# Performance work log

Measured on AMD Instinct MI355X. Metric: run time of the kernel, lower is better.

Reference implementation:

```python
import jax, jax.numpy as jnp
import numpy as np

R = 2            # interleaving factor (init kwarg r)
C = 16           # feature channels
N = 500_000      # number of sparse voxels
GRID = 256       # fine-grid extent per axis


def setup_inputs() -> dict:
    key = jax.random.key(0)
    kc, kf = jax.random.split(key)
    coords = jax.random.randint(kc, (N, 3), 0, GRID, dtype=jnp.int32)
    feats = jax.random.normal(kf, (N, C), dtype=jnp.float32)
    return {"feats": feats, "coords": coords}


def reference(feats, coords):
    # Sparse interleaving: group fine voxels into coarse voxels of size R^3,
    # scattering each point's C features into the slot given by its intra-cell offset.
    r2 = R * R
    r3 = r2 * R
    n = coords.shape[0]
    base = coords // R                      # [N,3] coarse voxel coords
    off = coords % R                        # [N,3] intra-cell offset
    offset_idx = off[:, 0] * r2 + off[:, 1] * R + off[:, 2]  # [N]

    # jit-compatible unique: fixed output size (worst case: all points distinct)
    unique_coords, inv = jnp.unique(base, axis=0, size=n, fill_value=-1,
                                    return_inverse=True)
    inv = inv.reshape(-1)                   # [N] row in aggregated output

    # target column = offset_idx*C + channel  (matches torch scatter_ layout)
    col = offset_idx[:, None] * C + jnp.arange(C, dtype=offset_idx.dtype)[None, :]  # [N,C]
    agg = jnp.zeros((n, C * r3), dtype=feats.dtype)
    agg = agg.at[inv[:, None], col].set(feats)
    return unique_coords.astype(jnp.int32), agg
```

## Files before the change

### kernel.cpp

```cpp
#include <hip/hip_runtime.h>


#define WORDS 65536u

__global__ void mark_kernel(const int* __restrict__ coords,
                            unsigned* __restrict__ bitmap, int n) {
    int i = blockIdx.x * 256 + threadIdx.x;
    if (i >= n) return;
    int cx = coords[3 * i], cy = coords[3 * i + 1], cz = coords[3 * i + 2];
    unsigned key = ((unsigned)(cx >> 1) << 14) | ((unsigned)(cy >> 1) << 7) |
                   (unsigned)(cz >> 1);
    atomicOr(&bitmap[key >> 5], 1u << (key & 31));
}

__global__ void scanall_kernel(const unsigned* __restrict__ bitmap,
                               unsigned* __restrict__ chunkExcl,
                               unsigned* __restrict__ U) {
    __shared__ unsigned sh[256];
    int t = threadIdx.x;
    unsigned s = 0;
    unsigned base = (unsigned)t * 256u;
#pragma unroll 8
    for (unsigned j = 0; j < 256u; ++j) s += __popc(bitmap[base + j]);
    unsigned x = s;
    sh[t] = x; __syncthreads();
    for (int d = 1; d < 256; d <<= 1) {
        unsigned y = (t >= d) ? sh[t - d] : 0u;
        __syncthreads();
        x += y; sh[t] = x; __syncthreads();
    }
    chunkExcl[t] = x - s;
    if (t == 255) *U = x;
}

__global__ void rank_coords_pad_kernel(const unsigned* __restrict__ bitmap,
                                       const unsigned* __restrict__ chunkExcl,
                                       const unsigned* __restrict__ U,
                                       unsigned* __restrict__ rank_base,
                                       float* __restrict__ coords_out, int n) {
    __shared__ unsigned sh[256];
    int t = threadIdx.x;
    unsigned w = blockIdx.x * 256 + t;
    unsigned word = bitmap[w];
    unsigned cnt = __popc(word);
    unsigned x = cnt;
    sh[t] = x; __syncthreads();
    for (int d = 1; d < 256; d <<= 1) {
        unsigned y = (t >= d) ? sh[t - d] : 0u;
        __syncthreads();
        x += y; sh[t] = x; __syncthreads();
    }
    unsigned rb = chunkExcl[blockIdx.x] + x - cnt;
    rank_base[w] = rb;
    while (word) {
        int k = __ffs(word) - 1;
        word &= word - 1;
        unsigned cell = w * 32u + (unsigned)k;
        coords_out[3 * rb + 0] = (float)(cell >> 14);
        coords_out[3 * rb + 1] = (float)((cell >> 7) & 127u);
        coords_out[3 * rb + 2] = (float)(cell & 127u);
        ++rb;
    }
    unsigned u = *U;
    int nthreads = gridDim.x * 256;
    for (unsigned i = u + w; i < (unsigned)n; i += nthreads) {
        coords_out[3 * i + 0] = -1.0f;
        coords_out[3 * i + 1] = -1.0f;
        coords_out[3 * i + 2] = -1.0f;
    }
}

__global__ void winner_kernel(const int* __restrict__ coords,
                              const unsigned* __restrict__ bitmap,
                              const unsigned* __restrict__ rank_base,
                              int* __restrict__ winner, int n) {
    int i = blockIdx.x * 256 + threadIdx.x;
    if (i >= n) return;
    int cx = coords[3 * i], cy = coords[3 * i + 1], cz = coords[3 * i + 2];
    unsigned key = ((unsigned)(cx >> 1) << 14) | ((unsigned)(cy >> 1) << 7) |
                   (unsigned)(cz >> 1);
    unsigned off = ((unsigned)(cx & 1) << 2) | ((unsigned)(cy & 1) << 1) |
                   (unsigned)(cz & 1);
    unsigned wd = key >> 5;
    unsigned r = rank_base[wd] + __popc(bitmap[wd] & ((1u << (key & 31)) - 1u));
    atomicMax(&winner[r * 8u + off], i);
}

__global__ void gather_kernel(const float* __restrict__ feats,
                              const int* __restrict__ winner,
                              float* __restrict__ agg, int total4) {
    int j = blockIdx.x * 256 + threadIdx.x;
    if (j >= total4) return;
    int slot = j >> 2;
    int c4 = j & 3;
    int w = winner[slot];
    float4 v = make_float4(0.f, 0.f, 0.f, 0.f);
    if (w >= 0) v = ((const float4*)feats)[(size_t)w * 4 + c4];
    ((float4*)agg)[j] = v;
}

extern "C" void kernel_launch(void* const* d_in, const int* in_sizes, int n_in,
                              void* d_out, int out_size, void* d_ws, size_t ws_size,
                              hipStream_t stream) {
    const float* feats = (const float*)d_in[0];
    const int* coords  = (const int*)d_in[1];
    int n = in_sizes[1] / 3;

    float* out        = (float*)d_out;
    float* coords_out = out;
    float* agg        = out + (size_t)3 * n;

    unsigned* bitmap    = (unsigned*)d_ws;
    unsigned* rank_base = bitmap + WORDS;
    unsigned* chunkExcl = rank_base + WORDS;
    unsigned* U         = chunkExcl + 256;
    int*      winner    = (int*)(U + 4);

    (void)hipMemsetAsync(bitmap, 0, WORDS * sizeof(unsigned), stream);

    int nb = (n + 255) / 256;
    mark_kernel<<<nb, 256, 0, stream>>>(coords, bitmap, n);
    scanall_kernel<<<1, 256, 0, stream>>>(bitmap, chunkExcl, U);
    rank_coords_pad_kernel<<<WORDS / 256, 256, 0, stream>>>(bitmap, chunkExcl, U,
                                                            rank_base, coords_out, n);
    winner_kernel<<<nb, 256, 0, stream>>>(coords, bitmap, rank_base, winner, n);
    int total4 = n * 32;
    gather_kernel<<<(total4 + 255) / 256, 256, 0, stream>>>(feats, winner, agg,
                                                            total4);
}
```

Before: 373.9 us.

## Fuse all interleave stages into one persistent kernel with grid barriers

Replaces the five separate launches (mark, scan, rank/coords, winner, gather) with one persistent kernel of 1024 blocks. The stages are separated by atomic-counter grid barriers, and all loops become grid-stride. The per-chunk popcount reduction is now spread over 256 blocks instead of one block doing a serial 256-word loop. This removes inter-kernel launch gaps and the single-block scan bottleneck. In exchange it relies on all 1024 blocks being co-resident for the spin barriers to avoid deadlock, and adds barrier synchronisation cost.

```diff
diff --git a/kernel.cpp b/kernel.cpp
--- a/kernel.cpp
+++ b/kernel.cpp
@@ -1,102 +1,128 @@
 #include <hip/hip_runtime.h>
 
 
-#define WORDS 65536u
+#define WORDS   65536u
+#define NBLK    1024u
+#define NTHREAD (NBLK * 256u)
 
-__global__ void mark_kernel(const int* __restrict__ coords,
-                            unsigned* __restrict__ bitmap, int n) {
-    int i = blockIdx.x * 256 + threadIdx.x;
-    if (i >= n) return;
-    int cx = coords[3 * i], cy = coords[3 * i + 1], cz = coords[3 * i + 2];
-    unsigned key = ((unsigned)(cx >> 1) << 14) | ((unsigned)(cy >> 1) << 7) |
-                   (unsigned)(cz >> 1);
-    atomicOr(&bitmap[key >> 5], 1u << (key & 31));
+__device__ __forceinline__ void gridbar(unsigned* ctr) {
+    __threadfence();
+    __syncthreads();
+    if (threadIdx.x == 0) {
+        atomicAdd(ctr, 1u);
+        while (__hip_atomic_load(ctr, __ATOMIC_ACQUIRE,
+                                 __HIP_MEMORY_SCOPE_AGENT) < NBLK)
+            __builtin_amdgcn_s_sleep(8);
+    }
+    __syncthreads();
+    __threadfence();
 }
 
-__global__ void scanall_kernel(const unsigned* __restrict__ bitmap,
-                               unsigned* __restrict__ chunkExcl,
-                               unsigned* __restrict__ U) {
+__global__ __launch_bounds__(256, 4)
+void interleave_fused(const float* __restrict__ feats,
+                      const int* __restrict__ coords,
+                      unsigned* __restrict__ ctrs,
+                      unsigned* __restrict__ bitmap,
+                      unsigned* __restrict__ chunkExcl,
+                      unsigned* __restrict__ Uptr,
+                      unsigned* __restrict__ rank_base,
+                      int* __restrict__ winner,
+                      float* __restrict__ coords_out,
+                      float* __restrict__ agg,
+                      int n) {
     __shared__ unsigned sh[256];
-    int t = threadIdx.x;
-    unsigned s = 0;
-    unsigned base = (unsigned)t * 256u;
-#pragma unroll 8
-    for (unsigned j = 0; j < 256u; ++j) s += __popc(bitmap[base + j]);
-    unsigned x = s;
-    sh[t] = x; __syncthreads();
-    for (int d = 1; d < 256; d <<= 1) {
-        unsigned y = (t >= d) ? sh[t - d] : 0u;
+    const int t   = threadIdx.x;
+    const int b   = blockIdx.x;
+    const int gid = b * 256 + t;
+
+    for (int i = gid; i < n; i += NTHREAD) {
+        int cx = coords[3 * i], cy = coords[3 * i + 1], cz = coords[3 * i + 2];
+        unsigned key = ((unsigned)(cx >> 1) << 14) | ((unsigned)(cy >> 1) << 7) |
+                       (unsigned)(cz >> 1);
+        atomicOr(&bitmap[key >> 5], 1u << (key & 31));
+    }
+    gridbar(&ctrs[0]);
+
+    if (b < 256) {
+        sh[t] = __popc(bitmap[b * 256 + t]);
         __syncthreads();
-        x += y; sh[t] = x; __syncthreads();
+        for (int d = 128; d > 0; d >>= 1) {
+            if (t < d) sh[t] += sh[t + d];
+            __syncthreads();
+        }
+        if (t == 0) chunkExcl[b] = sh[0];
     }
-    chunkExcl[t] = x - s;
-    if (t == 255) *U = x;
-}
+    gridbar(&ctrs[1]);
 
-__global__ void rank_coords_pad_kernel(const unsigned* __restrict__ bitmap,
-                                       const unsigned* __restrict__ chunkExcl,
-                                       const unsigned* __restrict__ U,
-                                       unsigned* __restrict__ rank_base,
-                                       float* __restrict__ coords_out, int n) {
-    __shared__ unsigned sh[256];
-    int t = threadIdx.x;
-    unsigned w = blockIdx.x * 256 + t;
-    unsigned word = bitmap[w];
-    unsigned cnt = __popc(word);
-    unsigned x = cnt;
-    sh[t] = x; __syncthreads();
-    for (int d = 1; d < 256; d <<= 1) {
-        unsigned y = (t >= d) ? sh[t - d] : 0u;
-        __syncthreads();
-        x += y; sh[t] = x; __syncthreads();
+    if (b == 0) {
+        unsigned s = chunkExcl[t];
+        unsigned x = s;
+        sh[t] = x; __syncthreads();
+        for (int d = 1; d < 256; d <<= 1) {
+            unsigned y = (t >= d) ? sh[t - d] : 0u;
+            __syncthreads();
+            x += y; sh[t] = x; __syncthreads();
+        }
+        chunkExcl[t] = x - s;
+        if (t == 255) *Uptr = x;
     }
-    unsigned rb = chunkExcl[blockIdx.x] + x - cnt;
-    rank_base[w] = rb;
-    while (word) {
-        int k = __ffs(word) - 1;
-        word &= word - 1;
-        unsigned cell = w * 32u + (unsigned)k;
-        coords_out[3 * rb + 0] = (float)(cell >> 14);
-        coords_out[3 * rb + 1] = (float)((cell >> 7) & 127u);
-        coords_out[3 * rb + 2] = (float)(cell & 127u);
-        ++rb;
+    gridbar(&ctrs[2]);
+
+    if (b < 256) {
+        unsigned w = b * 256 + t;
+        unsigned word = bitmap[w];
+        unsigned cnt = __popc(word);
+        unsigned x = cnt;
+        sh[t] = x; __syncthreads();
+        for (int d = 1; d < 256; d <<= 1) {
+            unsigned y = (t >= d) ? sh[t - d] : 0u;
+            __syncthreads();
+            x += y; sh[t] = x; __syncthreads();
+        }
+        unsigned rb = chunkExcl[b] + x - cnt;
+        rank_base[w] = rb;
+        while (word) {
+            int k = __ffs(word) - 1;
+            word &= word - 1;
+            unsigned cell = w * 32u + (unsigned)k;
+            coords_out[3 * rb + 0] = (float)(cell >> 14);
+            coords_out[3 * rb + 1] = (float)((cell >> 7) & 127u);
+            coords_out[3 * rb + 2] = (float)(cell & 127u);
+            ++rb;
+        }
     }
-    unsigned u = *U;
-    int nthreads = gridDim.x * 256;
-    for (unsigned i = u + w; i < (unsigned)n; i += nthreads) {
-        coords_out[3 * i + 0] = -1.0f;
-        coords_out[3 * i + 1] = -1.0f;
-        coords_out[3 * i + 2] = -1.0f;
+    {
+        unsigned u = *Uptr;
+        for (unsigned i = u + gid; i < (unsigned)n; i += NTHREAD) {
+            coords_out[3 * i + 0] = -1.0f;
+            coords_out[3 * i + 1] = -1.0f;
+            coords_out[3 * i + 2] = -1.0f;
+        }
     }
-}
+    gridbar(&ctrs[3]);
 
-__global__ void winner_kernel(const int* __restrict__ coords,
-                              const unsigned* __restrict__ bitmap,
-                              const unsigned* __restrict__ rank_base,
-                              int* __restrict__ winner, int n) {
-    int i = blockIdx.x * 256 + threadIdx.x;
-    if (i >= n) return;
-    int cx = coords[3 * i], cy = coords[3 * i + 1], cz = coords[3 * i + 2];
-    unsigned key = ((unsigned)(cx >> 1) << 14) | ((unsigned)(cy >> 1) << 7) |
-                   (unsigned)(cz >> 1);
-    unsigned off = ((unsigned)(cx & 1) << 2) | ((unsigned)(cy & 1) << 1) |
-                   (unsigned)(cz & 1);
-    unsigned wd = key >> 5;
-    unsigned r = rank_base[wd] + __popc(bitmap[wd] & ((1u << (key & 31)) - 1u));
-    atomicMax(&winner[r * 8u + off], i);
-}
+    for (int i = gid; i < n; i += NTHREAD) {
+        int cx = coords[3 * i], cy = coords[3 * i + 1], cz = coords[3 * i + 2];
+        unsigned key = ((unsigned)(cx >> 1) << 14) | ((unsigned)(cy >> 1) << 7) |
+                       (unsigned)(cz >> 1);
+        unsigned off = ((unsigned)(cx & 1) << 2) | ((unsigned)(cy & 1) << 1) |
+                       (unsigned)(cz & 1);
+        unsigned wd = key >> 5;
+        unsigned r = rank_base[wd] +
+                     __popc(bitmap[wd] & ((1u << (key & 31)) - 1u));
+        atomicMax(&winner[r * 8u + off], i);
+    }
+    gridbar(&ctrs[4]);
 
-__global__ void gather_kernel(const float* __restrict__ feats,
-                              const int* __restrict__ winner,
-                              float* __restrict__ agg, int total4) {
-    int j = blockIdx.x * 256 + threadIdx.x;
-    if (j >= total4) return;
-    int slot = j >> 2;
-    int c4 = j & 3;
-    int w = winner[slot];
-    float4 v = make_float4(0.f, 0.f, 0.f, 0.f);
-    if (w >= 0) v = ((const float4*)feats)[(size_t)w * 4 + c4];
-    ((float4*)agg)[j] = v;
+    int total4 = n * 32;
+    for (int j = gid; j < total4; j += NTHREAD) {
+        int slot = j >> 2;
+        int c4 = j & 3;
+        int w = winner[slot];
+        float4 v = make_float4(0.f, 0.f, 0.f, 0.f);
+        if (w >= 0) v = ((const float4*)feats)[(size_t)w * 4 + c4];
+        ((float4*)agg)[j] = v;
+    }
 }
 
 extern "C" void kernel_launch(void* const* d_in, const int* in_sizes, int n_in,
@@ -110,21 +136,16 @@
     float* coords_out = out;
     float* agg        = out + (size_t)3 * n;
 
-    unsigned* bitmap    = (unsigned*)d_ws;
-    unsigned* rank_base = bitmap + WORDS;
-    unsigned* chunkExcl = rank_base + WORDS;
+    unsigned* ctrs      = (unsigned*)d_ws;
+    unsigned* bitmap    = ctrs + 8;
+    unsigned* chunkExcl = bitmap + WORDS;
     unsigned* U         = chunkExcl + 256;
-    int*      winner    = (int*)(U + 4);
+    unsigned* rank_base = U + 4;
+    int*      winner    = (int*)(rank_base + WORDS);
 
-    (void)hipMemsetAsync(bitmap, 0, WORDS * sizeof(unsigned), stream);
+    (void)hipMemsetAsync(ctrs, 0, (8 + WORDS) * sizeof(unsigned), stream);
 
-    int nb = (n + 255) / 256;
-    mark_kernel<<<nb, 256, 0, stream>>>(coords, bitmap, n);
-    scanall_kernel<<<1, 256, 0, stream>>>(bitmap, chunkExcl, U);
-    rank_coords_pad_kernel<<<WORDS / 256, 256, 0, stream>>>(bitmap, chunkExcl, U,
-                                                            rank_base, coords_out, n);
-    winner_kernel<<<nb, 256, 0, stream>>>(coords, bitmap, rank_base, winner, n);
-    int total4 = n * 32;
-    gather_kernel<<<(total4 + 255) / 256, 256, 0, stream>>>(feats, winner, agg,
-                                                            total4);
+    interleave_fused<<<NBLK, 256, 0, stream>>>(feats, coords, ctrs, bitmap,
+                                               chunkExcl, U, rank_base, winner,
+                                               coords_out, agg, n);
 }
```

After: 1.350 ms. 261% more time.

## Replace per-slot gather with memset plus per-point scatter of winning features

Applied to the files above, without the earlier changes.

The final stage no longer gathers over every output slot. The whole aggregated output is zeroed with a bulk memset. Then a per-point kernel recomputes each point's slot and copies its 64-byte feature row only when it is the winning writer. This drops the full read of the winner array and the per-slot branching. In exchange it adds a second pass of coords, bitmap and rank lookups plus scattered 64-byte writes on top of the full-size memset.

```diff
diff --git a/kernel.cpp b/kernel.cpp
--- a/kernel.cpp
+++ b/kernel.cpp
@@ -86,17 +86,26 @@
     atomicMax(&winner[r * 8u + off], i);
 }
 
-__global__ void gather_kernel(const float* __restrict__ feats,
-                              const int* __restrict__ winner,
-                              float* __restrict__ agg, int total4) {
-    int j = blockIdx.x * 256 + threadIdx.x;
-    if (j >= total4) return;
-    int slot = j >> 2;
-    int c4 = j & 3;
-    int w = winner[slot];
-    float4 v = make_float4(0.f, 0.f, 0.f, 0.f);
-    if (w >= 0) v = ((const float4*)feats)[(size_t)w * 4 + c4];
-    ((float4*)agg)[j] = v;
+__global__ void scatter_kernel(const float* __restrict__ feats,
+                               const int* __restrict__ coords,
+                               const unsigned* __restrict__ bitmap,
+                               const unsigned* __restrict__ rank_base,
+                               const int* __restrict__ winner,
+                               float* __restrict__ agg, int n) {
+    int i = blockIdx.x * 256 + threadIdx.x;
+    if (i >= n) return;
+    int cx = coords[3 * i], cy = coords[3 * i + 1], cz = coords[3 * i + 2];
+    unsigned key = ((unsigned)(cx >> 1) << 14) | ((unsigned)(cy >> 1) << 7) |
+                   (unsigned)(cz >> 1);
+    unsigned off = ((unsigned)(cx & 1) << 2) | ((unsigned)(cy & 1) << 1) |
+                   (unsigned)(cz & 1);
+    unsigned wd = key >> 5;
+    unsigned r = rank_base[wd] + __popc(bitmap[wd] & ((1u << (key & 31)) - 1u));
+    unsigned slot = r * 8u + off;
+    if (winner[slot] != i) return;
+    const float4* src = (const float4*)(feats + (size_t)i * 16);
+    float4* dst = (float4*)(agg + (size_t)slot * 16u);
+    dst[0] = src[0]; dst[1] = src[1]; dst[2] = src[2]; dst[3] = src[3];
 }
 
 extern "C" void kernel_launch(void* const* d_in, const int* in_sizes, int n_in,
@@ -117,6 +126,7 @@
     int*      winner    = (int*)(U + 4);
 
     (void)hipMemsetAsync(bitmap, 0, WORDS * sizeof(unsigned), stream);
+    (void)hipMemsetAsync(agg, 0, (size_t)128 * n * sizeof(float), stream);
 
     int nb = (n + 255) / 256;
     mark_kernel<<<nb, 256, 0, stream>>>(coords, bitmap, n);
@@ -124,7 +134,6 @@
     rank_coords_pad_kernel<<<WORDS / 256, 256, 0, stream>>>(bitmap, chunkExcl, U,
                                                             rank_base, coords_out, n);
     winner_kernel<<<nb, 256, 0, stream>>>(coords, bitmap, rank_base, winner, n);
-    int total4 = n * 32;
-    gather_kernel<<<(total4 + 255) / 256, 256, 0, stream>>>(feats, winner, agg,
-                                                            total4);
+    scatter_kernel<<<nb, 256, 0, stream>>>(feats, coords, bitmap, rank_base,
+                                           winner, agg, n);
 }
```

Measured after the change: 416.9 us. 11.5% more time.
